# Kernel optimization log

Hardware: AMD Instinct MI355X
Metric: run time of the kernel (lower is better)

The kernel has to match this reference:

```python
import jax, jax.numpy as jnp
import numpy as np


def conv2d(x, w, b=None, pad=0):
    # x: [N,C,H,W], w: [O,I,kh,kw] (cross-correlation, matches torch conv2d)
    out = jax.lax.conv_general_dilated(
        x, w, window_strides=(1, 1), padding=[(pad, pad), (pad, pad)],
        dimension_numbers=('NCHW', 'OIHW', 'NCHW'))
    if b is not None:
        out = out + b[None, :, None, None]
    return out


def se_block(f, w1, b1, w2, b2):
    # squeeze-excite: global avg pool -> 1x1 conv -> relu -> 1x1 conv -> sigmoid
    s = jnp.mean(f, axis=(2, 3), keepdims=True)
    s = jax.nn.relu(conv2d(s, w1, b1, pad=0))
    s = jax.nn.sigmoid(conv2d(s, w2, b2, pad=0))
    return f * s


def setup_inputs() -> dict:
    key = jax.random.key(0)
    ks = jax.random.split(key, 32)
    B, C, H, W = 8, 3, 128, 128
    F_, S, K = 128, 8, 72  # features, squeeze, n basis kernels
    rn = lambda k, shp, sc=0.05: (jax.random.normal(k, shp, dtype=jnp.float32) * sc)
    return {
        'x': jax.random.normal(ks[0], (B, C, H, W), dtype=jnp.float32),
        'w_head': rn(ks[1], (F_, C, 3, 3)), 'b_head': rn(ks[2], (F_,)),
        'w_h1a': rn(ks[3], (F_, F_, 3, 3)), 'b_h1a': rn(ks[4], (F_,)),
        'w_h1b': rn(ks[5], (F_, F_, 3, 3)), 'b_h1b': rn(ks[6], (F_,)),
        'du1_w1': rn(ks[7], (S, F_, 1, 1)), 'du1_b1': rn(ks[8], (S,)),
        'du1_w2': rn(ks[9], (F_, S, 1, 1)), 'du1_b2': rn(ks[10], (F_,)),
        'w_h2a': rn(ks[11], (F_, F_, 3, 3)), 'b_h2a': rn(ks[12], (F_,)),
        'w_h2b': rn(ks[13], (F_, F_, 3, 3)), 'b_h2b': rn(ks[14], (F_,)),
        'du2_w1': rn(ks[15], (S, F_, 1, 1)), 'du2_b1': rn(ks[16], (S,)),
        'du2_w2': rn(ks[17], (F_, S, 1, 1)), 'du2_b2': rn(ks[18], (F_,)),
        'w_tail': rn(ks[19], (K, F_, 3, 3)), 'b_tail': rn(ks[20], (K,)),
        'kernel': rn(ks[21], (K, 1, 5, 5), 0.2),  # fixed 72x5x5 basis
    }


def reference(x, w_head, b_head, w_h1a, b_h1a, w_h1b, b_h1b,
              du1_w1, du1_b1, du1_w2, du1_b2,
              w_h2a, b_h2a, w_h2b, b_h2b,
              du2_w1, du2_b1, du2_w2, du2_b2,
              w_tail, b_tail, kernel):
    B, C, H, W = x.shape
    K = kernel.shape[0]
    # trunk: head -> (conv relu)x2 -> SE -> (conv relu)x2 -> SE -> tail
    f = conv2d(x, w_head, b_head, pad=1)
    f = jax.nn.relu(conv2d(f, w_h1a, b_h1a, pad=1))
    f = jax.nn.relu(conv2d(f, w_h1b, b_h1b, pad=1))
    f = se_block(f, du1_w1, du1_b1, du1_w2, du1_b2)
    f = jax.nn.relu(conv2d(f, w_h2a, b_h2a, pad=1))
    f = jax.nn.relu(conv2d(f, w_h2b, b_h2b, pad=1))
    f = se_block(f, du2_w1, du2_b1, du2_w2, du2_b2)
    wgt = conv2d(f, w_tail, b_tail, pad=1).reshape(B, 1, K, H, W)
    # dynamic filtering: apply 72 fixed 5x5 basis kernels per channel, then
    # per-pixel weighted sum over the 72 basis responses
    xp = jnp.pad(x, ((0, 0), (0, 0), (2, 2), (2, 2)), mode='reflect')
    xp = xp.reshape(B * C, 1, H + 4, W + 4)
    x_com = conv2d(xp, kernel, None, pad=0).reshape(B, C, K, H, W)
    out = jnp.sum(wgt * x_com, axis=2)  # [B,3,H,W]
    return out
```

## Files before the change

### kernel.cpp

```cpp
#include <hip/hip_runtime.h>
#include <math.h>


typedef __attribute__((ext_vector_type(8))) short bf16x8;
typedef __attribute__((ext_vector_type(4))) float f32x4;

__device__ inline float bf2f(unsigned short u) {
    unsigned v = ((unsigned)u) << 16;
    return __builtin_bit_cast(float, v);
}
__device__ inline unsigned short f2bf(float f) {
    unsigned u = __builtin_bit_cast(unsigned, f);
    u += 0x7FFF + ((u >> 16) & 1);
    return (unsigned short)(u >> 16);
}

__global__ __launch_bounds__(256) void head_conv(
    const float* __restrict__ x, const float* __restrict__ w,
    const float* __restrict__ bias, unsigned short* __restrict__ out)
{
    __shared__ float wlds[216];
    __shared__ float tile[3][34 * 34];
    const int tid = threadIdx.x, cog = blockIdx.y, b = blockIdx.z;
    const int tile_y = (blockIdx.x >> 2) * 32, tile_x = (blockIdx.x & 3) * 32;

    if (tid < 216) {
        int co = tid & 7, rest = tid >> 3, tap = rest % 9, ci = rest / 9;
        wlds[tid] = w[((cog * 8 + co) * 3 + ci) * 9 + tap];
    }
    for (int idx = tid; idx < 3 * 34 * 34; idx += 256) {
        int ci = idx / 1156, rem = idx - ci * 1156;
        int r = rem / 34, c = rem - r * 34;
        int gy = tile_y - 1 + r, gx = tile_x - 1 + c;
        float v = 0.f;
        if ((unsigned)gy < 128u && (unsigned)gx < 128u)
            v = x[(((size_t)(b * 3 + ci)) << 14) + (gy << 7) + gx];
        tile[ci][rem] = v;
    }
    __syncthreads();

    const int ty = tid >> 4, tx = tid & 15, py = ty * 2;
    float acc[2][2][8];
    #pragma unroll
    for (int r = 0; r < 2; ++r)
        #pragma unroll
        for (int h = 0; h < 2; ++h)
            #pragma unroll
            for (int co = 0; co < 8; ++co) acc[r][h][co] = 0.f;

    #pragma unroll
    for (int ci = 0; ci < 3; ++ci) {
        #pragma unroll
        for (int ky = 0; ky < 3; ++ky) {
            #pragma unroll
            for (int kx = 0; kx < 3; ++kx) {
                const float* wp = wlds + (ci * 9 + ky * 3 + kx) * 8;
                float i00 = tile[ci][(py + ky) * 34 + tx + kx];
                float i01 = tile[ci][(py + ky) * 34 + tx + 16 + kx];
                float i10 = tile[ci][(py + 1 + ky) * 34 + tx + kx];
                float i11 = tile[ci][(py + 1 + ky) * 34 + tx + 16 + kx];
                #pragma unroll
                for (int co = 0; co < 8; ++co) {
                    float wv = wp[co];
                    acc[0][0][co] += i00 * wv;
                    acc[0][1][co] += i01 * wv;
                    acc[1][0][co] += i10 * wv;
                    acc[1][1][co] += i11 * wv;
                }
            }
        }
    }

    #pragma unroll
    for (int r = 0; r < 2; ++r) {
        #pragma unroll
        for (int h = 0; h < 2; ++h) {
            int gy = tile_y + py + r, gx = tile_x + tx + h * 16;
            bf16x8 pv;
            #pragma unroll
            for (int co = 0; co < 8; ++co)
                pv[co] = (short)f2bf(acc[r][h][co] + bias[cog * 8 + co]);
            *(bf16x8*)(out + (((((size_t)b << 14) + gy * 128 + gx)) << 7) + cog * 8) = pv;
        }
    }
}

template <int LM, int NTW, int NSPLIT>
__global__ __launch_bounds__(256, 2) void conv_mfma(
    const unsigned short* __restrict__ in, const unsigned short* __restrict__ wT,
    size_t wstride, const float* __restrict__ bias, unsigned short* __restrict__ out,
    int Coutp, int Cout, int relu)
{
    __shared__ unsigned short lds[324 * 72];
    const int tid = threadIdx.x;
    const int b = blockIdx.y;
    const int row0 = (blockIdx.x >> 3) << 4;
    const int col0 = (blockIdx.x & 7) << 4;
    const int l = tid & 63, wv = tid >> 6;
    const int li = l & 15, lq = l >> 4;
    const int m_base = NSPLIT ? (wv >> 1) * LM : wv * LM;
    const int n_base = NSPLIT ? (wv & 1) * NTW : 0;
    const size_t inb = ((size_t)b) << 14;
    const unsigned short* wbase = wT + (size_t)b * wstride;

    f32x4 acc[LM][NTW];
    #pragma unroll
    for (int lm = 0; lm < LM; ++lm)
        #pragma unroll
        for (int nt = 0; nt < NTW; ++nt)
            acc[lm][nt] = (f32x4){0.f, 0.f, 0.f, 0.f};

    #pragma unroll 1
    for (int half = 0; half < 2; ++half) {
        __syncthreads();
        for (int u = tid; u < 2592; u += 256) {
            int px = u >> 3, part = u & 7;
            int hr = px / 18, hc = px - hr * 18;
            int gy = row0 - 1 + hr, gx = col0 - 1 + hc;
            bf16x8 v = {0, 0, 0, 0, 0, 0, 0, 0};
            if ((unsigned)gy < 128u && (unsigned)gx < 128u)
                v = *(const bf16x8*)(in + ((inb + (gy << 7) + gx) << 7) + half * 64 + part * 8);
            *(bf16x8*)(lds + px * 72 + part * 8) = v;
        }
        __syncthreads();

        auto loadB = [&](bf16x8 (&dst)[NTW], int s) {
            int tap = s >> 1, kcl = s & 1;
            const unsigned short* p = wbase +
                (size_t)(tap * 4 + half * 2 + kcl) * (Coutp * 32) +
                (n_base * 16 + li) * 32 + lq * 8;
            #pragma unroll
            for (int nt = 0; nt < NTW; ++nt)
                dst[nt] = *(const bf16x8*)(p + nt * 512);
        };
        auto compute = [&](bf16x8 (&bf)[NTW], int s) {
            int tap = s >> 1, kcl = s & 1;
            int ky = tap / 3, kx = tap - ky * 3;
            int coff = kcl * 32 + lq * 8;
            #pragma unroll
            for (int lm = 0; lm < LM; ++lm) {
                bf16x8 af = *(const bf16x8*)(
                    lds + ((m_base + lm + ky) * 18 + li + kx) * 72 + coff);
                #pragma unroll
                for (int nt = 0; nt < NTW; ++nt)
                    acc[lm][nt] = __builtin_amdgcn_mfma_f32_16x16x32_bf16(
                        af, bf[nt], acc[lm][nt], 0, 0, 0);
            }
        };

        bf16x8 bufA[NTW], bufB[NTW];
        loadB(bufA, 0);
        #pragma unroll 1
        for (int it = 0; it < 18; it += 2) {
            loadB(bufB, it + 1);
            compute(bufA, it);
            if (it + 2 < 18) loadB(bufA, it + 2);
            compute(bufB, it + 1);
        }
    }

    float bv[NTW];
    #pragma unroll
    for (int nt = 0; nt < NTW; ++nt) {
        int co = (n_base + nt) * 16 + li;
        bv[nt] = (co < Cout) ? bias[co] : 0.f;
    }
    #pragma unroll
    for (int lm = 0; lm < LM; ++lm) {
        int row = row0 + m_base + lm;
        #pragma unroll
        for (int r = 0; r < 4; ++r) {
            int col = col0 + lq * 4 + r;
            size_t pbase = (inb + row * 128 + col) * (size_t)Coutp;
            #pragma unroll
            for (int nt = 0; nt < NTW; ++nt) {
                float v = acc[lm][nt][r] + bv[nt];
                if (relu) v = fmaxf(v, 0.f);
                out[pbase + (n_base + nt) * 16 + li] = f2bf(v);
            }
        }
    }
}

__global__ __launch_bounds__(256) void wtrans(
    const float* __restrict__ w, unsigned short* __restrict__ wT, int Co, int Coutp)
{
    int idx = blockIdx.x * 256 + threadIdx.x;
    if (idx >= 9 * 4 * Coutp * 32) return;
    int ch = idx & 31;
    int rest = idx >> 5;
    int co = rest % Coutp;
    int slice = rest / Coutp;
    int kc = slice & 3, tap = slice >> 2;
    float v = (co < Co) ? w[((size_t)(co * 128 + kc * 32 + ch)) * 9 + tap] : 0.f;
    wT[idx] = f2bf(v);
}

__global__ __launch_bounds__(256) void wscale8(
    const unsigned short* __restrict__ wT, const float* __restrict__ scale,
    unsigned short* __restrict__ out, int Coutp)
{
    int r = blockIdx.x * 256 + threadIdx.x;
    int b = blockIdx.y;
    int ch = r & 31;
    int slice = (r >> 5) / Coutp;
    int kc = slice & 3;
    float s = scale[b * 128 + kc * 32 + ch];
    out[(size_t)b * (9 * 4 * Coutp * 32) + r] = f2bf(bf2f(wT[r]) * s);
}

__global__ __launch_bounds__(256) void mean_nhwc(
    const unsigned short* __restrict__ f, float* __restrict__ meanb)
{
    const int b = blockIdx.y, slab = blockIdx.x;
    const int p = threadIdx.x >> 4, g = threadIdx.x & 15;
    const size_t base = ((size_t)b << 14) + slab * 256;

    float s[8] = {0.f, 0.f, 0.f, 0.f, 0.f, 0.f, 0.f, 0.f};
    #pragma unroll
    for (int i = 0; i < 16; ++i) {
        bf16x8 v = *(const bf16x8*)(f + ((base + p + i * 16) << 7) + g * 8);
        #pragma unroll
        for (int j = 0; j < 8; ++j) s[j] += bf2f((unsigned short)v[j]);
    }

    __shared__ float tmp[16][16][8];
    #pragma unroll
    for (int j = 0; j < 8; ++j) tmp[p][g][j] = s[j];
    __syncthreads();
    if (threadIdx.x < 128) {
        int ch = threadIdx.x;
        float t = 0.f;
        #pragma unroll
        for (int pp = 0; pp < 16; ++pp) t += tmp[pp][ch >> 3][ch & 7];
        atomicAdd(&meanb[b * 128 + ch], t);
    }
}

__global__ __launch_bounds__(128) void se_kernel(
    const float* __restrict__ meanb, const float* __restrict__ w1,
    const float* __restrict__ b1, const float* __restrict__ w2,
    const float* __restrict__ b2, float* __restrict__ scale)
{
    const int b = blockIdx.x, c = threadIdx.x;
    __shared__ float h1[8];
    if (c < 8) {
        float s = 0.f;
        for (int j = 0; j < 128; ++j) s += w1[c * 128 + j] * meanb[b * 128 + j];
        h1[c] = fmaxf(s * (1.f / 16384.f) + b1[c], 0.f);
    }
    __syncthreads();
    float s = b2[c];
    #pragma unroll
    for (int j = 0; j < 8; ++j) s += w2[c * 8 + j] * h1[j];
    scale[b * 128 + c] = 1.f / (1.f + expf(-s));
}

__global__ __launch_bounds__(256) void dynfilter(
    const float* __restrict__ x, const unsigned short* __restrict__ wgt,
    const float* __restrict__ kern, float* __restrict__ out)
{
    __shared__ unsigned short wl[256 * 88];
    const int blk = blockIdx.x;
    const int b = blk >> 6;
    const int px0 = (blk & 63) << 8;

    const unsigned short* src = wgt + ((size_t)b * 16384 + px0) * 80;
    for (int u = threadIdx.x; u < 2560; u += 256) {
        int px = u / 10, k8 = u - px * 10;
        *(bf16x8*)(wl + px * 88 + k8 * 8) = *(const bf16x8*)(src + u * 8);
    }
    __syncthreads();

    const int pix = px0 + threadIdx.x;
    const int h = pix >> 7, w = pix & 127;
    const unsigned short* rowp = wl + threadIdx.x * 88;

    float e[25];
    #pragma unroll
    for (int i = 0; i < 25; ++i) e[i] = 0.f;
    #pragma unroll
    for (int u8 = 0; u8 < 9; ++u8) {
        bf16x8 wv8 = *(const bf16x8*)(rowp + u8 * 8);
        #pragma unroll
        for (int j = 0; j < 8; ++j) {
            float wk = bf2f((unsigned short)wv8[j]);
            const float* kp = kern + (u8 * 8 + j) * 25;
            #pragma unroll
            for (int i = 0; i < 25; ++i) e[i] += wk * kp[i];
        }
    }

    int yy[5], xx[5];
    #pragma unroll
    for (int d = 0; d < 5; ++d) {
        int y = h - 2 + d;
        yy[d] = y < 0 ? -y : (y > 127 ? 254 - y : y);
        int xv = w - 2 + d;
        xx[d] = xv < 0 ? -xv : (xv > 127 ? 254 - xv : xv);
    }

    #pragma unroll
    for (int c = 0; c < 3; ++c) {
        const float* xc = x + ((size_t)(b * 3 + c) << 14);
        float s = 0.f;
        #pragma unroll
        for (int dy = 0; dy < 5; ++dy)
            #pragma unroll
            for (int dx = 0; dx < 5; ++dx)
                s += e[dy * 5 + dx] * xc[yy[dy] * 128 + xx[dx]];
        out[((size_t)(b * 3 + c) << 14) + pix] = s;
    }
}

extern "C" void kernel_launch(void* const* d_in, const int* in_sizes, int n_in,
                              void* d_out, int out_size, void* d_ws, size_t ws_size,
                              hipStream_t stream)
{
    const float* x      = (const float*)d_in[0];
    const float* w_head = (const float*)d_in[1];
    const float* b_head = (const float*)d_in[2];
    const float* w_h1a  = (const float*)d_in[3];
    const float* b_h1a  = (const float*)d_in[4];
    const float* w_h1b  = (const float*)d_in[5];
    const float* b_h1b  = (const float*)d_in[6];
    const float* du1_w1 = (const float*)d_in[7];
    const float* du1_b1 = (const float*)d_in[8];
    const float* du1_w2 = (const float*)d_in[9];
    const float* du1_b2 = (const float*)d_in[10];
    const float* w_h2a  = (const float*)d_in[11];
    const float* b_h2a  = (const float*)d_in[12];
    const float* w_h2b  = (const float*)d_in[13];
    const float* b_h2b  = (const float*)d_in[14];
    const float* du2_w1 = (const float*)d_in[15];
    const float* du2_b1 = (const float*)d_in[16];
    const float* du2_w2 = (const float*)d_in[17];
    const float* du2_b2 = (const float*)d_in[18];
    const float* w_tail = (const float*)d_in[19];
    const float* b_tail = (const float*)d_in[20];
    const float* kern   = (const float*)d_in[21];
    float* out = (float*)d_out;

    unsigned short* fb0  = (unsigned short*)d_ws;
    unsigned short* fb1  = fb0 + 16777216;
    unsigned short* wgtb = fb1 + 16777216;
    unsigned short* wt1  = wgtb + 10485760;
    unsigned short* wt2  = wt1 + 147456;
    unsigned short* wt3  = wt2 + 147456;
    unsigned short* wt4  = wt3 + 147456;
    unsigned short* wtt  = wt4 + 147456;
    unsigned short* wsa  = wtt + 92160;
    unsigned short* wst  = wsa + 8 * 147456;
    float* meanb  = (float*)(wst + 8 * 92160);
    float* scaleb = meanb + 1024;

    dim3 blk(256);
    wtrans<<<576, blk, 0, stream>>>(w_h1a, wt1, 128, 128);
    wtrans<<<576, blk, 0, stream>>>(w_h1b, wt2, 128, 128);
    wtrans<<<576, blk, 0, stream>>>(w_h2a, wt3, 128, 128);
    wtrans<<<576, blk, 0, stream>>>(w_h2b, wt4, 128, 128);
    wtrans<<<360, blk, 0, stream>>>(w_tail, wtt, 72, 80);

    head_conv<<<dim3(16, 16, 8), blk, 0, stream>>>(x, w_head, b_head, fb0);

    dim3 cgrid(64, 8);
    conv_mfma<8, 4, 1><<<cgrid, blk, 0, stream>>>(fb0, wt1, 0, b_h1a, fb1, 128, 128, 1);
    conv_mfma<8, 4, 1><<<cgrid, blk, 0, stream>>>(fb1, wt2, 0, b_h1b, fb0, 128, 128, 1);

    hipMemsetAsync(meanb, 0, 4096, stream);
    mean_nhwc<<<dim3(64, 8), blk, 0, stream>>>(fb0, meanb);
    se_kernel<<<8, 128, 0, stream>>>(meanb, du1_w1, du1_b1, du1_w2, du1_b2, scaleb);
    wscale8<<<dim3(576, 8), blk, 0, stream>>>(wt3, scaleb, wsa, 128);

    conv_mfma<8, 4, 1><<<cgrid, blk, 0, stream>>>(fb0, wsa, 147456, b_h2a, fb1, 128, 128, 1);
    conv_mfma<8, 4, 1><<<cgrid, blk, 0, stream>>>(fb1, wt4, 0, b_h2b, fb0, 128, 128, 1);

    hipMemsetAsync(meanb, 0, 4096, stream);
    mean_nhwc<<<dim3(64, 8), blk, 0, stream>>>(fb0, meanb);
    se_kernel<<<8, 128, 0, stream>>>(meanb, du2_w1, du2_b1, du2_w2, du2_b2, scaleb);
    wscale8<<<dim3(360, 8), blk, 0, stream>>>(wtt, scaleb, wst, 80);

    conv_mfma<4, 5, 0><<<cgrid, blk, 0, stream>>>(fb0, wst, 92160, b_tail, wgtb, 80, 72, 0);

    dynfilter<<<512, blk, 0, stream>>>(x, wgtb, kern, out);
}
```

Measured before the change: 375.9 us.

## Fuse SE channel mean into conv epilogue and halve conv tile height

Removes the separate mean_nhwc reduction kernels by accumulating per-channel sums in the second conv's epilogue and adding them to a global buffer with atomics after a wave shuffle. A single memset up front clears both mean buffers. The conv tile also shrinks from 16x16 to 8x16 pixels, doubling the grid and raising the launch-bounds occupancy hint from 2 to 3 blocks per CU. Smaller tiles mean more halo reloads and more weight traffic per output pixel, and the means are now summed from fp32 values before bf16 rounding rather than from the stored bf16 features.

```diff
diff --git a/kernel.cpp b/kernel.cpp
--- a/kernel.cpp
+++ b/kernel.cpp
@@ -85,16 +85,16 @@
     }
 }
 
-template <int LM, int NTW, int NSPLIT>
-__global__ __launch_bounds__(256, 2) void conv_mfma(
+template <int LM, int NTW, int NSPLIT, int DOMEAN>
+__global__ __launch_bounds__(256, 3) void conv_mfma(
     const unsigned short* __restrict__ in, const unsigned short* __restrict__ wT,
     size_t wstride, const float* __restrict__ bias, unsigned short* __restrict__ out,
-    int Coutp, int Cout, int relu)
-{
-    __shared__ unsigned short lds[324 * 72];
+    float* __restrict__ meanb, int Coutp, int Cout, int relu)
+{
+    __shared__ unsigned short lds[180 * 72];
     const int tid = threadIdx.x;
     const int b = blockIdx.y;
-    const int row0 = (blockIdx.x >> 3) << 4;
+    const int row0 = (blockIdx.x >> 3) << 3;
     const int col0 = (blockIdx.x & 7) << 4;
     const int l = tid & 63, wv = tid >> 6;
     const int li = l & 15, lq = l >> 4;
@@ -113,7 +113,7 @@
     #pragma unroll 1
     for (int half = 0; half < 2; ++half) {
         __syncthreads();
-        for (int u = tid; u < 2592; u += 256) {
+        for (int u = tid; u < 1440; u += 256) {
             int px = u >> 3, part = u & 7;
             int hr = px / 18, hc = px - hr * 18;
             int gy = row0 - 1 + hr, gx = col0 - 1 + hc;
@@ -159,11 +159,12 @@
         }
     }
 
-    float bv[NTW];
+    float bv[NTW], msum[NTW];
     #pragma unroll
     for (int nt = 0; nt < NTW; ++nt) {
         int co = (n_base + nt) * 16 + li;
         bv[nt] = (co < Cout) ? bias[co] : 0.f;
+        msum[nt] = 0.f;
     }
     #pragma unroll
     for (int lm = 0; lm < LM; ++lm) {
@@ -176,8 +177,19 @@
             for (int nt = 0; nt < NTW; ++nt) {
                 float v = acc[lm][nt][r] + bv[nt];
                 if (relu) v = fmaxf(v, 0.f);
+                if (DOMEAN) msum[nt] += v;
                 out[pbase + (n_base + nt) * 16 + li] = f2bf(v);
             }
+        }
+    }
+    if (DOMEAN) {
+        #pragma unroll
+        for (int nt = 0; nt < NTW; ++nt) {
+            float t = msum[nt];
+            t += __shfl_xor(t, 16, 64);
+            t += __shfl_xor(t, 32, 64);
+            if (lq == 0)
+                atomicAdd(&meanb[b * 128 + (n_base + nt) * 16 + li], t);
         }
     }
 }
@@ -207,34 +219,6 @@
     int kc = slice & 3;
     float s = scale[b * 128 + kc * 32 + ch];
     out[(size_t)b * (9 * 4 * Coutp * 32) + r] = f2bf(bf2f(wT[r]) * s);
-}
-
-__global__ __launch_bounds__(256) void mean_nhwc(
-    const unsigned short* __restrict__ f, float* __restrict__ meanb)
-{
-    const int b = blockIdx.y, slab = blockIdx.x;
-    const int p = threadIdx.x >> 4, g = threadIdx.x & 15;
-    const size_t base = ((size_t)b << 14) + slab * 256;
-
-    float s[8] = {0.f, 0.f, 0.f, 0.f, 0.f, 0.f, 0.f, 0.f};
-    #pragma unroll
-    for (int i = 0; i < 16; ++i) {
-        bf16x8 v = *(const bf16x8*)(f + ((base + p + i * 16) << 7) + g * 8);
-        #pragma unroll
-        for (int j = 0; j < 8; ++j) s[j] += bf2f((unsigned short)v[j]);
-    }
-
-    __shared__ float tmp[16][16][8];
-    #pragma unroll
-    for (int j = 0; j < 8; ++j) tmp[p][g][j] = s[j];
-    __syncthreads();
-    if (threadIdx.x < 128) {
-        int ch = threadIdx.x;
-        float t = 0.f;
-        #pragma unroll
-        for (int pp = 0; pp < 16; ++pp) t += tmp[pp][ch >> 3][ch & 7];
-        atomicAdd(&meanb[b * 128 + ch], t);
-    }
 }
 
 __global__ __launch_bounds__(128) void se_kernel(
@@ -351,10 +335,13 @@
     unsigned short* wtt  = wt4 + 147456;
     unsigned short* wsa  = wtt + 92160;
     unsigned short* wst  = wsa + 8 * 147456;
-    float* meanb  = (float*)(wst + 8 * 92160);
-    float* scaleb = meanb + 1024;
+    float* mean1  = (float*)(wst + 8 * 92160);
+    float* mean2  = mean1 + 1024;
+    float* scaleb = mean2 + 1024;
 
     dim3 blk(256);
+    hipMemsetAsync(mean1, 0, 8192, stream);
+
     wtrans<<<576, blk, 0, stream>>>(w_h1a, wt1, 128, 128);
     wtrans<<<576, blk, 0, stream>>>(w_h1b, wt2, 128, 128);
     wtrans<<<576, blk, 0, stream>>>(w_h2a, wt3, 128, 128);
@@ -363,24 +350,20 @@
 
     head_conv<<<dim3(16, 16, 8), blk, 0, stream>>>(x, w_head, b_head, fb0);
 
-    dim3 cgrid(64, 8);
-    conv_mfma<8, 4, 1><<<cgrid, blk, 0, stream>>>(fb0, wt1, 0, b_h1a, fb1, 128, 128, 1);
-    conv_mfma<8, 4, 1><<<cgrid, blk, 0, stream>>>(fb1, wt2, 0, b_h1b, fb0, 128, 128, 1);
-
-    hipMemsetAsync(meanb, 0, 4096, stream);
-    mean_nhwc<<<dim3(64, 8), blk, 0, stream>>>(fb0, meanb);
-    se_kernel<<<8, 128, 0, stream>>>(meanb, du1_w1, du1_b1, du1_w2, du1_b2, scaleb);
+    dim3 cgrid(128, 8);
+    conv_mfma<4, 4, 1, 0><<<cgrid, blk, 0, stream>>>(fb0, wt1, 0, b_h1a, fb1, nullptr, 128, 128, 1);
+    conv_mfma<4, 4, 1, 1><<<cgrid, blk, 0, stream>>>(fb1, wt2, 0, b_h1b, fb0, mean1, 128, 128, 1);
+
+    se_kernel<<<8, 128, 0, stream>>>(mean1, du1_w1, du1_b1, du1_w2, du1_b2, scaleb);
     wscale8<<<dim3(576, 8), blk, 0, stream>>>(wt3, scaleb, wsa, 128);
 
-    conv_mfma<8, 4, 1><<<cgrid, blk, 0, stream>>>(fb0, wsa, 147456, b_h2a, fb1, 128, 128, 1);
-    conv_mfma<8, 4, 1><<<cgrid, blk, 0, stream>>>(fb1, wt4, 0, b_h2b, fb0, 128, 128, 1);
-
-    hipMemsetAsync(meanb, 0, 4096, stream);
-    mean_nhwc<<<dim3(64, 8), blk, 0, stream>>>(fb0, meanb);
-    se_kernel<<<8, 128, 0, stream>>>(meanb, du2_w1, du2_b1, du2_w2, du2_b2, scaleb);
+    conv_mfma<4, 4, 1, 0><<<cgrid, blk, 0, stream>>>(fb0, wsa, 147456, b_h2a, fb1, nullptr, 128, 128, 1);
+    conv_mfma<4, 4, 1, 1><<<cgrid, blk, 0, stream>>>(fb1, wt4, 0, b_h2b, fb0, mean2, 128, 128, 1);
+
+    se_kernel<<<8, 128, 0, stream>>>(mean2, du2_w1, du2_b1, du2_w2, du2_b2, scaleb);
     wscale8<<<dim3(360, 8), blk, 0, stream>>>(wtt, scaleb, wst, 80);
 
-    conv_mfma<4, 5, 0><<<cgrid, blk, 0, stream>>>(fb0, wst, 92160, b_tail, wgtb, 80, 72, 0);
+    conv_mfma<2, 5, 0, 0><<<cgrid, blk, 0, stream>>>(fb0, wst, 92160, b_tail, wgtb, nullptr, 80, 72, 0);
 
     dynfilter<<<512, blk, 0, stream>>>(x, wgtb, kern, out);
 }
```

Result: slower. 478.1 us (+27.2%).
